# Kernel optimization log

Measured on AMD Instinct MI355X. Metric: run time of the kernel, lower is better.

The kernel has to match this reference:

```python
import jax, jax.numpy as jnp
import numpy as np

B, T, D, H = 4, 1024, 1024, 16
DH = D // H  # 64

def setup_inputs() -> dict:
    key = jax.random.key(0)
    ks = jax.random.split(key, 5)
    s = 1.0 / np.sqrt(D)
    return {
        "x": jax.random.normal(ks[0], (B, T, D), dtype=jnp.float32),
        "Wqkv": jax.random.uniform(ks[1], (D, 3 * D), dtype=jnp.float32, minval=-s, maxval=s),
        "bqkv": jax.random.uniform(ks[2], (3 * D,), dtype=jnp.float32, minval=-s, maxval=s),
        "Wproj": jax.random.uniform(ks[3], (D, D), dtype=jnp.float32, minval=-s, maxval=s),
        "bproj": jax.random.uniform(ks[4], (D,), dtype=jnp.float32, minval=-s, maxval=s),
        "mask": jnp.ones((B, T), dtype=jnp.int32),
    }

def reference(x, Wqkv, bqkv, Wproj, bproj, mask):
    Bx, Tx, C = x.shape
    qkv = x @ Wqkv + bqkv                      # [B,T,3D]
    q, k, v = jnp.split(qkv, 3, axis=-1)
    # [B,H,T,DH]
    q = q.reshape(Bx, Tx, H, DH).transpose(0, 2, 1, 3)
    k = k.reshape(Bx, Tx, H, DH).transpose(0, 2, 1, 3)
    v = v.reshape(Bx, Tx, H, DH).transpose(0, 2, 1, 3)
    att = jnp.einsum("bhqd,bhkd->bhqk", q, k) / np.sqrt(DH)
    causal = jnp.tril(jnp.ones((Tx, Tx), dtype=bool))          # [T,T]
    keep = causal[None, None] & (mask[:, None, None, :] != 0)  # [B,1,T,T] broadcast
    att = jnp.where(keep, att, -jnp.inf)
    att = jax.nn.softmax(att, axis=-1)
    # dropout is identity in eval / p=0
    out = jnp.einsum("bhqk,bhkd->bhqd", att, v)                # [B,H,T,DH]
    out = out.transpose(0, 2, 1, 3).reshape(Bx, Tx, C)
    return out @ Wproj + bproj
```

## Files before the change

### kernel.cpp

```cpp
#include <hip/hip_runtime.h>
#include <hip/hip_bf16.h>
#include <cstddef>
#include <cstdint>

#define Bb 4
#define Tt 1024
#define Dd 1024
#define Hh 16

typedef __bf16 bf16x8 __attribute__((ext_vector_type(8)));
typedef __bf16 bf16x4 __attribute__((ext_vector_type(4)));
typedef float  f32x4  __attribute__((ext_vector_type(4)));

__device__ __forceinline__ void gload16(const void* g, void* l) {
    __builtin_amdgcn_global_load_lds(
        (const __attribute__((address_space(1))) void*)g,
        (__attribute__((address_space(3))) void*)l, 16, 0, 0);
}

__global__ __launch_bounds__(256) void cast_f32_bf16(const float* __restrict__ in,
                                                     __bf16* __restrict__ out, int n4) {
    int i = blockIdx.x * 256 + threadIdx.x;
    if (i < n4) {
        float4 v = ((const float4*)in)[i];
        bf16x4 o = { (__bf16)v.x, (__bf16)v.y, (__bf16)v.z, (__bf16)v.w };
        ((bf16x4*)out)[i] = o;
    }
}

__global__ __launch_bounds__(256) void transpose_cast(const float* __restrict__ in,
                                                      __bf16* __restrict__ out,
                                                      int K, int N) {
    __shared__ float ld[64][65];
    const int k0 = blockIdx.x * 64;
    const int n0 = blockIdx.y * 64;
    #pragma unroll
    for (int i = 0; i < 16; i++) {
        int idx = i * 256 + threadIdx.x;
        int r = idx >> 6, c = idx & 63;
        ld[r][c] = in[(size_t)(k0 + r) * N + n0 + c];
    }
    __syncthreads();
    #pragma unroll
    for (int i = 0; i < 16; i++) {
        int idx = i * 256 + threadIdx.x;
        int r = idx >> 6, c = idx & 63;
        out[(size_t)(n0 + r) * K + k0 + c] = (__bf16)ld[c][r];
    }
}

__global__ __launch_bounds__(256) void gemm_bf16(const __bf16* __restrict__ A,
                                                 const __bf16* __restrict__ Bt,
                                                 const float* __restrict__ bias,
                                                 void* __restrict__ Cout,
                                                 __bf16* __restrict__ vtout,
                                                 int M, int N, int K, int mode) {
    __shared__ __align__(16) __bf16 As[128 * 32];
    __shared__ __align__(16) __bf16 Bs[128 * 32];
    const int tid  = threadIdx.x;
    const int lane = tid & 63;
    const int wave = tid >> 6;
    const int wy = wave >> 1, wx = wave & 1;
    const int l15 = lane & 15, quad = lane >> 4;
    const size_t row0 = (size_t)blockIdx.y * 128;
    const size_t col0 = (size_t)blockIdx.x * 128;

    f32x4 acc[4][4] = {};

    for (int k0 = 0; k0 < K; k0 += 32) {
        #pragma unroll
        for (int i = 0; i < 2; i++) {
            int chunk = i * 256 + tid;
            int r = chunk >> 2, seg = chunk & 3;
            gload16(&A[(row0 + r) * K + k0 + seg * 8], &As[chunk * 8]);
        }
        #pragma unroll
        for (int i = 0; i < 2; i++) {
            int chunk = i * 256 + tid;
            int r = chunk >> 2, seg = chunk & 3;
            gload16(&Bt[(col0 + r) * K + k0 + seg * 8], &Bs[chunk * 8]);
        }
        __syncthreads();
        bf16x8 af[4], bfr[4];
        #pragma unroll
        for (int i = 0; i < 4; i++)
            af[i] = *(const bf16x8*)&As[(wy * 64 + i * 16 + l15) * 32 + quad * 8];
        #pragma unroll
        for (int j = 0; j < 4; j++)
            bfr[j] = *(const bf16x8*)&Bs[(wx * 64 + j * 16 + l15) * 32 + quad * 8];
        #pragma unroll
        for (int i = 0; i < 4; i++)
            #pragma unroll
            for (int j = 0; j < 4; j++)
                acc[i][j] = __builtin_amdgcn_mfma_f32_16x16x32_bf16(af[i], bfr[j], acc[i][j], 0, 0, 0);
        __syncthreads();
    }

    #pragma unroll
    for (int j = 0; j < 4; j++) {
        const size_t col = col0 + wx * 64 + j * 16 + l15;
        const float bj = bias[col];
        const float scale = (mode == 1 && col < 1024) ? 0.125f : 1.0f;
        #pragma unroll
        for (int i = 0; i < 4; i++) {
            const size_t row = row0 + wy * 64 + i * 16 + quad * 4;
            #pragma unroll
            for (int r = 0; r < 4; r++) {
                float v = (acc[i][j][r] + bj) * scale;
                if (mode == 1) {
                    __bf16 bv_ = (__bf16)v;
                    ((__bf16*)Cout)[(row + r) * N + col] = bv_;
                    if (col >= 2048) {
                        size_t rw = row + r;
                        int bidx = (int)(rw >> 10), t = (int)(rw & 1023);
                        int hd = (int)col - 2048;
                        vtout[((size_t)((bidx * Hh + (hd >> 6)) * 64 + (hd & 63))) * Tt + t] = bv_;
                    }
                } else {
                    ((float*)Cout)[(row + r) * N + col] = v;
                }
            }
        }
    }
}

__global__ __launch_bounds__(256) void gemm_bf16_n64(const __bf16* __restrict__ A,
                                                     const __bf16* __restrict__ Bt,
                                                     const float* __restrict__ bias,
                                                     float* __restrict__ Cout,
                                                     int M, int N, int K) {
    __shared__ __align__(16) __bf16 As[128 * 32];
    __shared__ __align__(16) __bf16 Bs[64 * 32];
    const int tid  = threadIdx.x;
    const int lane = tid & 63;
    const int wave = tid >> 6;
    const int wy = wave >> 1, wx = wave & 1;
    const int l15 = lane & 15, quad = lane >> 4;
    const size_t row0 = (size_t)blockIdx.y * 128;
    const size_t col0 = (size_t)blockIdx.x * 64;

    f32x4 acc[4][2] = {};

    for (int k0 = 0; k0 < K; k0 += 32) {
        #pragma unroll
        for (int i = 0; i < 2; i++) {
            int chunk = i * 256 + tid;
            int r = chunk >> 2, seg = chunk & 3;
            gload16(&A[(row0 + r) * K + k0 + seg * 8], &As[chunk * 8]);
        }
        {
            int chunk = tid;
            int r = chunk >> 2, seg = chunk & 3;
            gload16(&Bt[(col0 + r) * K + k0 + seg * 8], &Bs[chunk * 8]);
        }
        __syncthreads();
        bf16x8 af[4], bfr[2];
        #pragma unroll
        for (int i = 0; i < 4; i++)
            af[i] = *(const bf16x8*)&As[(wy * 64 + i * 16 + l15) * 32 + quad * 8];
        #pragma unroll
        for (int j = 0; j < 2; j++)
            bfr[j] = *(const bf16x8*)&Bs[(wx * 32 + j * 16 + l15) * 32 + quad * 8];
        #pragma unroll
        for (int i = 0; i < 4; i++)
            #pragma unroll
            for (int j = 0; j < 2; j++)
                acc[i][j] = __builtin_amdgcn_mfma_f32_16x16x32_bf16(af[i], bfr[j], acc[i][j], 0, 0, 0);
        __syncthreads();
    }

    #pragma unroll
    for (int j = 0; j < 2; j++) {
        const size_t col = col0 + wx * 32 + j * 16 + l15;
        const float bj = bias[col];
        #pragma unroll
        for (int i = 0; i < 4; i++) {
            const size_t row = row0 + wy * 64 + i * 16 + quad * 4;
            #pragma unroll
            for (int r = 0; r < 4; r++)
                Cout[(row + r) * N + col] = acc[i][j][r] + bj;
        }
    }
}

__global__ __launch_bounds__(256, 2) void attn_mfma(const __bf16* __restrict__ qkv,
                                                    const __bf16* __restrict__ vt,
                                                    const int* __restrict__ mask,
                                                    __bf16* __restrict__ att) {
    __shared__ __align__(16) __bf16 Qs[128 * 64];
    __shared__ __align__(16) __bf16 Ks[2][64 * 64];
    __shared__ __align__(16) __bf16 Vs[2][64 * 64];
    __shared__ __align__(16) __bf16 Ps[4][16 * 64];

    const int p = blockIdx.x, h = blockIdx.y, b = blockIdx.z;
    const int qlo = p, qhi = 15 - p, nk = 16 - p;
    const int tid = threadIdx.x, lane = tid & 63, wave = tid >> 6;
    const int l15 = lane & 15, quad = lane >> 4;

    #pragma unroll
    for (int i = 0; i < 4; i++) {
        int c = i * 256 + tid;
        int rr = c >> 3, ch = c & 7;
        int w_ = rr >> 5, s_ = (rr >> 4) & 1, r16 = rr & 15;
        int grow = (s_ ? qhi : qlo) * 64 + w_ * 16 + r16;
        gload16(&qkv[((size_t)(b * Tt + grow)) * 3072 + h * 64 + ((ch ^ (rr & 7)) * 8)],
                &Qs[c * 8]);
    }
    #pragma unroll
    for (int i = 0; i < 2; i++) {
        int c = i * 256 + tid;
        int rr = c >> 3, ch = c & 7, sw = (ch ^ (rr & 7)) * 8;
        gload16(&qkv[((size_t)(b * Tt + rr)) * 3072 + 1024 + h * 64 + sw], &Ks[0][c * 8]);
        gload16(&vt[((size_t)((b * Hh + h) * 64 + rr)) * Tt + sw], &Vs[0][c * 8]);
    }

    f32x4 Oacc[2][4] = {};
    f32x4 lacc[2] = {};
    bf16x8 ones;
    #pragma unroll
    for (int i = 0; i < 8; i++) ones[i] = (__bf16)1.0f;

    for (int kt = 0; kt < nk; kt++) {
        __syncthreads();
        const int cur = kt & 1;
        if (kt + 1 < nk) {
            #pragma unroll
            for (int i = 0; i < 2; i++) {
                int c = i * 256 + tid;
                int rr = c >> 3, ch = c & 7, sw = (ch ^ (rr & 7)) * 8;
                gload16(&qkv[((size_t)(b * Tt + (kt + 1) * 64 + rr)) * 3072 + 1024 + h * 64 + sw],
                        &Ks[cur ^ 1][c * 8]);
                gload16(&vt[((size_t)((b * Hh + h) * 64 + rr)) * Tt + (kt + 1) * 64 + sw],
                        &Vs[cur ^ 1][c * 8]);
            }
        }
        int mv[4];
        #pragma unroll
        for (int j = 0; j < 4; j++) mv[j] = mask[b * Tt + kt * 64 + j * 16 + l15];

        bf16x8 bk[4][2], bv[4][2];
        #pragma unroll
        for (int j = 0; j < 4; j++)
            #pragma unroll
            for (int kc = 0; kc < 2; kc++) {
                int sw = ((kc * 4 + quad) ^ (l15 & 7)) * 8;
                bk[j][kc] = *(const bf16x8*)&Ks[cur][(j * 16 + l15) * 64 + sw];
                bv[j][kc] = *(const bf16x8*)&Vs[cur][(j * 16 + l15) * 64 + sw];
            }

        #pragma unroll
        for (int s = 1; s >= 0; s--) {
            if (s == 0 && kt > qlo) continue;
            const int tile = s ? qhi : qlo;
            const int rowbase = wave * 32 + s * 16;
            bf16x8 aq0 = *(const bf16x8*)&Qs[(rowbase + l15) * 64 + ((quad ^ (l15 & 7)) * 8)];
            bf16x8 aq1 = *(const bf16x8*)&Qs[(rowbase + l15) * 64 + (((4 + quad) ^ (l15 & 7)) * 8)];
            #pragma unroll
            for (int j = 0; j < 4; j++) {
                f32x4 sa = {};
                sa = __builtin_amdgcn_mfma_f32_16x16x32_bf16(aq0, bk[j][0], sa, 0, 0, 0);
                sa = __builtin_amdgcn_mfma_f32_16x16x32_bf16(aq1, bk[j][1], sa, 0, 0, 0);
                #pragma unroll
                for (int r = 0; r < 4; r++) {
                    bool keep = (mv[j] != 0);
                    if (kt == tile) keep = keep && (j * 16 + l15 <= wave * 16 + quad * 4 + r);
                    float pe = keep ? __expf(sa[r]) : 0.0f;
                    int row = quad * 4 + r;
                    int chs = ((j * 2 + (l15 >> 3)) ^ (row & 7)) * 8 + (l15 & 7);
                    Ps[wave][row * 64 + chs] = (__bf16)pe;
                }
            }
            bf16x8 ap0 = *(const bf16x8*)&Ps[wave][l15 * 64 + ((quad ^ (l15 & 7)) * 8)];
            bf16x8 ap1 = *(const bf16x8*)&Ps[wave][l15 * 64 + (((4 + quad) ^ (l15 & 7)) * 8)];
            #pragma unroll
            for (int n = 0; n < 4; n++) {
                Oacc[s][n] = __builtin_amdgcn_mfma_f32_16x16x32_bf16(ap0, bv[n][0], Oacc[s][n], 0, 0, 0);
                Oacc[s][n] = __builtin_amdgcn_mfma_f32_16x16x32_bf16(ap1, bv[n][1], Oacc[s][n], 0, 0, 0);
            }
            lacc[s] = __builtin_amdgcn_mfma_f32_16x16x32_bf16(ap0, ones, lacc[s], 0, 0, 0);
            lacc[s] = __builtin_amdgcn_mfma_f32_16x16x32_bf16(ap1, ones, lacc[s], 0, 0, 0);
        }
    }

    #pragma unroll
    for (int s = 0; s < 2; s++) {
        const int tile = s ? qhi : qlo;
        #pragma unroll
        for (int r = 0; r < 4; r++) {
            const int grow = tile * 64 + wave * 16 + quad * 4 + r;
            const float inv = 1.0f / lacc[s][r];
            #pragma unroll
            for (int n = 0; n < 4; n++)
                att[((size_t)(b * Tt + grow)) * Dd + h * 64 + n * 16 + l15] =
                    (__bf16)(Oacc[s][n][r] * inv);
        }
    }
}

extern "C" void kernel_launch(void* const* d_in, const int* in_sizes, int n_in,
                              void* d_out, int out_size, void* d_ws, size_t ws_size,
                              hipStream_t stream) {
    const float* x     = (const float*)d_in[0];
    const float* Wqkv  = (const float*)d_in[1];
    const float* bqkv  = (const float*)d_in[2];
    const float* Wproj = (const float*)d_in[3];
    const float* bproj = (const float*)d_in[4];
    const int*   mask  = (const int*)d_in[5];
    float* out = (float*)d_out;

    __bf16* xb  = (__bf16*)d_ws;
    __bf16* wqT = xb  + (size_t)4096 * 1024;
    __bf16* wpT = wqT + (size_t)3072 * 1024;
    __bf16* qkv = wpT + (size_t)1024 * 1024;
    __bf16* vt  = qkv + (size_t)4096 * 3072;
    __bf16* att = vt  + (size_t)4 * 16 * 64 * 1024;

    cast_f32_bf16<<<4096, 256, 0, stream>>>(x, xb, (4096 * 1024) / 4);
    transpose_cast<<<dim3(16, 48), 256, 0, stream>>>(Wqkv, wqT, 1024, 3072);
    transpose_cast<<<dim3(16, 16), 256, 0, stream>>>(Wproj, wpT, 1024, 1024);

    gemm_bf16<<<dim3(24, 32), 256, 0, stream>>>(xb, wqT, bqkv, qkv, vt, 4096, 3072, 1024, 1);

    attn_mfma<<<dim3(8, 16, 4), 256, 0, stream>>>(qkv, vt, mask, att);

    gemm_bf16_n64<<<dim3(16, 32), 256, 0, stream>>>(att, wpT, bproj, out, 4096, 1024, 1024);
}
```

Measured before the change: 186.7 us.

## Widen GEMM K-tile with swizzled LDS, split V transpose, transpose attention MFMAs

Both GEMMs now stage 64-wide K tiles in XOR-swizzled LDS. This halves the barrier count per K and avoids bank conflicts on the fragment reads. The scattered V-transpose stores move out of the QKV GEMM epilogue into a separate LDS-tiled transpose kernel. The attention kernel swaps MFMA operand order so P stays in row layout, replaces the ones-matrix MFMA row sum with a register sum plus shuffles, and uses vector mask loads and vector output stores. These changes add one kernel launch and double LDS use in the GEMMs.

```diff
diff --git a/kernel.cpp b/kernel.cpp
--- a/kernel.cpp
+++ b/kernel.cpp
@@ -49,14 +49,36 @@
     }
 }
 
+__global__ __launch_bounds__(256) void v_transpose(const __bf16* __restrict__ qkv,
+                                                   __bf16* __restrict__ vt) {
+    __shared__ __bf16 ld[64][65];
+    const int t0 = blockIdx.x * 64;
+    const int h  = blockIdx.y;
+    const int b  = blockIdx.z;
+    const size_t src = ((size_t)(b * Tt + t0)) * 3072 + 2048 + h * 64;
+    #pragma unroll
+    for (int i = 0; i < 16; i++) {
+        int idx = i * 256 + threadIdx.x;
+        int tr = idx >> 6, dc = idx & 63;
+        ld[tr][dc] = qkv[src + (size_t)tr * 3072 + dc];
+    }
+    __syncthreads();
+    const size_t dst = ((size_t)((b * Hh + h) * 64)) * Tt + t0;
+    #pragma unroll
+    for (int i = 0; i < 16; i++) {
+        int idx = i * 256 + threadIdx.x;
+        int dr = idx >> 6, tc = idx & 63;
+        vt[dst + (size_t)dr * Tt + tc] = ld[tc][dr];
+    }
+}
+
 __global__ __launch_bounds__(256) void gemm_bf16(const __bf16* __restrict__ A,
                                                  const __bf16* __restrict__ Bt,
                                                  const float* __restrict__ bias,
                                                  void* __restrict__ Cout,
-                                                 __bf16* __restrict__ vtout,
                                                  int M, int N, int K, int mode) {
-    __shared__ __align__(16) __bf16 As[128 * 32];
-    __shared__ __align__(16) __bf16 Bs[128 * 32];
+    __shared__ __align__(16) __bf16 As[128 * 64];
+    __shared__ __align__(16) __bf16 Bs[128 * 64];
     const int tid  = threadIdx.x;
     const int lane = tid & 63;
     const int wave = tid >> 6;
@@ -67,32 +89,37 @@
 
     f32x4 acc[4][4] = {};
 
-    for (int k0 = 0; k0 < K; k0 += 32) {
-        #pragma unroll
-        for (int i = 0; i < 2; i++) {
-            int chunk = i * 256 + tid;
-            int r = chunk >> 2, seg = chunk & 3;
-            gload16(&A[(row0 + r) * K + k0 + seg * 8], &As[chunk * 8]);
-        }
-        #pragma unroll
-        for (int i = 0; i < 2; i++) {
-            int chunk = i * 256 + tid;
-            int r = chunk >> 2, seg = chunk & 3;
-            gload16(&Bt[(col0 + r) * K + k0 + seg * 8], &Bs[chunk * 8]);
-        }
-        __syncthreads();
-        bf16x8 af[4], bfr[4];
-        #pragma unroll
-        for (int i = 0; i < 4; i++)
-            af[i] = *(const bf16x8*)&As[(wy * 64 + i * 16 + l15) * 32 + quad * 8];
-        #pragma unroll
-        for (int j = 0; j < 4; j++)
-            bfr[j] = *(const bf16x8*)&Bs[(wx * 64 + j * 16 + l15) * 32 + quad * 8];
-        #pragma unroll
-        for (int i = 0; i < 4; i++)
+    for (int k0 = 0; k0 < K; k0 += 64) {
+        #pragma unroll
+        for (int i = 0; i < 4; i++) {
+            int c = i * 256 + tid;
+            int r = c >> 3, seg = (c & 7) ^ (r & 7);
+            gload16(&A[(row0 + r) * K + k0 + seg * 8], &As[c * 8]);
+        }
+        #pragma unroll
+        for (int i = 0; i < 4; i++) {
+            int c = i * 256 + tid;
+            int r = c >> 3, seg = (c & 7) ^ (r & 7);
+            gload16(&Bt[(col0 + r) * K + k0 + seg * 8], &Bs[c * 8]);
+        }
+        __syncthreads();
+        #pragma unroll
+        for (int kc = 0; kc < 2; kc++) {
+            bf16x8 af[4], bfr[4];
+            #pragma unroll
+            for (int i = 0; i < 4; i++)
+                af[i] = *(const bf16x8*)&As[(wy * 64 + i * 16 + l15) * 64 +
+                                            (((kc * 4 + quad) ^ (l15 & 7)) * 8)];
             #pragma unroll
             for (int j = 0; j < 4; j++)
-                acc[i][j] = __builtin_amdgcn_mfma_f32_16x16x32_bf16(af[i], bfr[j], acc[i][j], 0, 0, 0);
+                bfr[j] = *(const bf16x8*)&Bs[(wx * 64 + j * 16 + l15) * 64 +
+                                             (((kc * 4 + quad) ^ (l15 & 7)) * 8)];
+            #pragma unroll
+            for (int i = 0; i < 4; i++)
+                #pragma unroll
+                for (int j = 0; j < 4; j++)
+                    acc[i][j] = __builtin_amdgcn_mfma_f32_16x16x32_bf16(af[i], bfr[j], acc[i][j], 0, 0, 0);
+        }
         __syncthreads();
     }
 
@@ -107,18 +134,8 @@
             #pragma unroll
             for (int r = 0; r < 4; r++) {
                 float v = (acc[i][j][r] + bj) * scale;
-                if (mode == 1) {
-                    __bf16 bv_ = (__bf16)v;
-                    ((__bf16*)Cout)[(row + r) * N + col] = bv_;
-                    if (col >= 2048) {
-                        size_t rw = row + r;
-                        int bidx = (int)(rw >> 10), t = (int)(rw & 1023);
-                        int hd = (int)col - 2048;
-                        vtout[((size_t)((bidx * Hh + (hd >> 6)) * 64 + (hd & 63))) * Tt + t] = bv_;
-                    }
-                } else {
-                    ((float*)Cout)[(row + r) * N + col] = v;
-                }
+                if (mode == 1) ((__bf16*)Cout)[(row + r) * N + col] = (__bf16)v;
+                else           ((float*)Cout)[(row + r) * N + col] = v;
             }
         }
     }
@@ -129,8 +146,8 @@
                                                      const float* __restrict__ bias,
                                                      float* __restrict__ Cout,
                                                      int M, int N, int K) {
-    __shared__ __align__(16) __bf16 As[128 * 32];
-    __shared__ __align__(16) __bf16 Bs[64 * 32];
+    __shared__ __align__(16) __bf16 As[128 * 64];
+    __shared__ __align__(16) __bf16 Bs[64 * 64];
     const int tid  = threadIdx.x;
     const int lane = tid & 63;
     const int wave = tid >> 6;
@@ -141,31 +158,37 @@
 
     f32x4 acc[4][2] = {};
 
-    for (int k0 = 0; k0 < K; k0 += 32) {
+    for (int k0 = 0; k0 < K; k0 += 64) {
+        #pragma unroll
+        for (int i = 0; i < 4; i++) {
+            int c = i * 256 + tid;
+            int r = c >> 3, seg = (c & 7) ^ (r & 7);
+            gload16(&A[(row0 + r) * K + k0 + seg * 8], &As[c * 8]);
+        }
         #pragma unroll
         for (int i = 0; i < 2; i++) {
-            int chunk = i * 256 + tid;
-            int r = chunk >> 2, seg = chunk & 3;
-            gload16(&A[(row0 + r) * K + k0 + seg * 8], &As[chunk * 8]);
-        }
-        {
-            int chunk = tid;
-            int r = chunk >> 2, seg = chunk & 3;
-            gload16(&Bt[(col0 + r) * K + k0 + seg * 8], &Bs[chunk * 8]);
-        }
-        __syncthreads();
-        bf16x8 af[4], bfr[2];
-        #pragma unroll
-        for (int i = 0; i < 4; i++)
-            af[i] = *(const bf16x8*)&As[(wy * 64 + i * 16 + l15) * 32 + quad * 8];
-        #pragma unroll
-        for (int j = 0; j < 2; j++)
-            bfr[j] = *(const bf16x8*)&Bs[(wx * 32 + j * 16 + l15) * 32 + quad * 8];
-        #pragma unroll
-        for (int i = 0; i < 4; i++)
+            int c = i * 256 + tid;
+            int r = c >> 3, seg = (c & 7) ^ (r & 7);
+            gload16(&Bt[(col0 + r) * K + k0 + seg * 8], &Bs[c * 8]);
+        }
+        __syncthreads();
+        #pragma unroll
+        for (int kc = 0; kc < 2; kc++) {
+            bf16x8 af[4], bfr[2];
+            #pragma unroll
+            for (int i = 0; i < 4; i++)
+                af[i] = *(const bf16x8*)&As[(wy * 64 + i * 16 + l15) * 64 +
+                                            (((kc * 4 + quad) ^ (l15 & 7)) * 8)];
             #pragma unroll
             for (int j = 0; j < 2; j++)
-                acc[i][j] = __builtin_amdgcn_mfma_f32_16x16x32_bf16(af[i], bfr[j], acc[i][j], 0, 0, 0);
+                bfr[j] = *(const bf16x8*)&Bs[(wx * 32 + j * 16 + l15) * 64 +
+                                             (((kc * 4 + quad) ^ (l15 & 7)) * 8)];
+            #pragma unroll
+            for (int i = 0; i < 4; i++)
+                #pragma unroll
+                for (int j = 0; j < 2; j++)
+                    acc[i][j] = __builtin_amdgcn_mfma_f32_16x16x32_bf16(af[i], bfr[j], acc[i][j], 0, 0, 0);
+        }
         __syncthreads();
     }
 
@@ -209,16 +232,13 @@
     #pragma unroll
     for (int i = 0; i < 2; i++) {
         int c = i * 256 + tid;
-        int rr = c >> 3, ch = c & 7, sw = (ch ^ (rr & 7)) * 8;
+        int rr = c >> 3, ch = c & 7, sw = ((ch ^ (rr & 7)) * 8);
         gload16(&qkv[((size_t)(b * Tt + rr)) * 3072 + 1024 + h * 64 + sw], &Ks[0][c * 8]);
         gload16(&vt[((size_t)((b * Hh + h) * 64 + rr)) * Tt + sw], &Vs[0][c * 8]);
     }
 
     f32x4 Oacc[2][4] = {};
-    f32x4 lacc[2] = {};
-    bf16x8 ones;
-    #pragma unroll
-    for (int i = 0; i < 8; i++) ones[i] = (__bf16)1.0f;
+    float lsum[2] = { 0.0f, 0.0f };
 
     for (int kt = 0; kt < nk; kt++) {
         __syncthreads();
@@ -227,25 +247,29 @@
             #pragma unroll
             for (int i = 0; i < 2; i++) {
                 int c = i * 256 + tid;
-                int rr = c >> 3, ch = c & 7, sw = (ch ^ (rr & 7)) * 8;
+                int rr = c >> 3, ch = c & 7, sw = ((ch ^ (rr & 7)) * 8);
                 gload16(&qkv[((size_t)(b * Tt + (kt + 1) * 64 + rr)) * 3072 + 1024 + h * 64 + sw],
                         &Ks[cur ^ 1][c * 8]);
                 gload16(&vt[((size_t)((b * Hh + h) * 64 + rr)) * Tt + (kt + 1) * 64 + sw],
                         &Vs[cur ^ 1][c * 8]);
             }
         }
-        int mv[4];
-        #pragma unroll
-        for (int j = 0; j < 4; j++) mv[j] = mask[b * Tt + kt * 64 + j * 16 + l15];
-
-        bf16x8 bk[4][2], bv[4][2];
+
+        int mv4[4][4];
+        #pragma unroll
+        for (int j = 0; j < 4; j++) {
+            const int4 m4 = *(const int4*)&mask[b * Tt + kt * 64 + j * 16 + quad * 4];
+            mv4[j][0] = m4.x; mv4[j][1] = m4.y; mv4[j][2] = m4.z; mv4[j][3] = m4.w;
+        }
+
+        bf16x8 ak[4][2], av[4][2];
         #pragma unroll
         for (int j = 0; j < 4; j++)
             #pragma unroll
             for (int kc = 0; kc < 2; kc++) {
-                int sw = ((kc * 4 + quad) ^ (l15 & 7)) * 8;
-                bk[j][kc] = *(const bf16x8*)&Ks[cur][(j * 16 + l15) * 64 + sw];
-                bv[j][kc] = *(const bf16x8*)&Vs[cur][(j * 16 + l15) * 64 + sw];
+                int sw = (((kc * 4 + quad) ^ (l15 & 7)) * 8);
+                ak[j][kc] = *(const bf16x8*)&Ks[cur][(j * 16 + l15) * 64 + sw];
+                av[j][kc] = *(const bf16x8*)&Vs[cur][(j * 16 + l15) * 64 + sw];
             }
 
         #pragma unroll
@@ -253,46 +277,50 @@
             if (s == 0 && kt > qlo) continue;
             const int tile = s ? qhi : qlo;
             const int rowbase = wave * 32 + s * 16;
-            bf16x8 aq0 = *(const bf16x8*)&Qs[(rowbase + l15) * 64 + ((quad ^ (l15 & 7)) * 8)];
-            bf16x8 aq1 = *(const bf16x8*)&Qs[(rowbase + l15) * 64 + (((4 + quad) ^ (l15 & 7)) * 8)];
+            bf16x8 q0 = *(const bf16x8*)&Qs[(rowbase + l15) * 64 + ((quad ^ (l15 & 7)) * 8)];
+            bf16x8 q1 = *(const bf16x8*)&Qs[(rowbase + l15) * 64 + (((4 + quad) ^ (l15 & 7)) * 8)];
+
             #pragma unroll
             for (int j = 0; j < 4; j++) {
-                f32x4 sa = {};
-                sa = __builtin_amdgcn_mfma_f32_16x16x32_bf16(aq0, bk[j][0], sa, 0, 0, 0);
-                sa = __builtin_amdgcn_mfma_f32_16x16x32_bf16(aq1, bk[j][1], sa, 0, 0, 0);
+                f32x4 st = {};
+                st = __builtin_amdgcn_mfma_f32_16x16x32_bf16(ak[j][0], q0, st, 0, 0, 0);
+                st = __builtin_amdgcn_mfma_f32_16x16x32_bf16(ak[j][1], q1, st, 0, 0, 0);
+                bf16x4 pv;
                 #pragma unroll
                 for (int r = 0; r < 4; r++) {
-                    bool keep = (mv[j] != 0);
-                    if (kt == tile) keep = keep && (j * 16 + l15 <= wave * 16 + quad * 4 + r);
-                    float pe = keep ? __expf(sa[r]) : 0.0f;
-                    int row = quad * 4 + r;
-                    int chs = ((j * 2 + (l15 >> 3)) ^ (row & 7)) * 8 + (l15 & 7);
-                    Ps[wave][row * 64 + chs] = (__bf16)pe;
+                    const int tloc = j * 16 + quad * 4 + r;
+                    bool keep = (mv4[j][r] != 0);
+                    if (kt == tile) keep = keep && (tloc <= wave * 16 + l15);
+                    const float pe = keep ? __expf(st[r]) : 0.0f;
+                    lsum[s] += pe;
+                    pv[r] = (__bf16)pe;
                 }
-            }
-            bf16x8 ap0 = *(const bf16x8*)&Ps[wave][l15 * 64 + ((quad ^ (l15 & 7)) * 8)];
-            bf16x8 ap1 = *(const bf16x8*)&Ps[wave][l15 * 64 + (((4 + quad) ^ (l15 & 7)) * 8)];
+                *(bf16x4*)&Ps[wave][l15 * 64 + (((j * 4 + quad) ^ ((l15 & 7) << 1)) * 4)] = pv;
+            }
+            bf16x8 p0 = *(const bf16x8*)&Ps[wave][l15 * 64 + (((2 * quad) ^ ((l15 & 7) << 1)) * 4)];
+            bf16x8 p1 = *(const bf16x8*)&Ps[wave][l15 * 64 + (((2 * (4 + quad)) ^ ((l15 & 7) << 1)) * 4)];
             #pragma unroll
             for (int n = 0; n < 4; n++) {
-                Oacc[s][n] = __builtin_amdgcn_mfma_f32_16x16x32_bf16(ap0, bv[n][0], Oacc[s][n], 0, 0, 0);
-                Oacc[s][n] = __builtin_amdgcn_mfma_f32_16x16x32_bf16(ap1, bv[n][1], Oacc[s][n], 0, 0, 0);
-            }
-            lacc[s] = __builtin_amdgcn_mfma_f32_16x16x32_bf16(ap0, ones, lacc[s], 0, 0, 0);
-            lacc[s] = __builtin_amdgcn_mfma_f32_16x16x32_bf16(ap1, ones, lacc[s], 0, 0, 0);
+                Oacc[s][n] = __builtin_amdgcn_mfma_f32_16x16x32_bf16(av[n][0], p0, Oacc[s][n], 0, 0, 0);
+                Oacc[s][n] = __builtin_amdgcn_mfma_f32_16x16x32_bf16(av[n][1], p1, Oacc[s][n], 0, 0, 0);
+            }
         }
     }
 
     #pragma unroll
     for (int s = 0; s < 2; s++) {
         const int tile = s ? qhi : qlo;
-        #pragma unroll
-        for (int r = 0; r < 4; r++) {
-            const int grow = tile * 64 + wave * 16 + quad * 4 + r;
-            const float inv = 1.0f / lacc[s][r];
-            #pragma unroll
-            for (int n = 0; n < 4; n++)
-                att[((size_t)(b * Tt + grow)) * Dd + h * 64 + n * 16 + l15] =
-                    (__bf16)(Oacc[s][n][r] * inv);
+        float lt = lsum[s];
+        lt += __shfl_xor(lt, 16);
+        lt += __shfl_xor(lt, 32);
+        const float inv = 1.0f / lt;
+        const int q = tile * 64 + wave * 16 + l15;
+        #pragma unroll
+        for (int n = 0; n < 4; n++) {
+            bf16x4 o;
+            #pragma unroll
+            for (int r = 0; r < 4; r++) o[r] = (__bf16)(Oacc[s][n][r] * inv);
+            *(bf16x4*)&att[((size_t)(b * Tt + q)) * Dd + h * 64 + n * 16 + quad * 4] = o;
         }
     }
 }
@@ -319,8 +347,9 @@
     transpose_cast<<<dim3(16, 48), 256, 0, stream>>>(Wqkv, wqT, 1024, 3072);
     transpose_cast<<<dim3(16, 16), 256, 0, stream>>>(Wproj, wpT, 1024, 1024);
 
-    gemm_bf16<<<dim3(24, 32), 256, 0, stream>>>(xb, wqT, bqkv, qkv, vt, 4096, 3072, 1024, 1);
-
+    gemm_bf16<<<dim3(24, 32), 256, 0, stream>>>(xb, wqT, bqkv, qkv, 4096, 3072, 1024, 1);
+
+    v_transpose<<<dim3(16, 16, 4), 256, 0, stream>>>(qkv, vt);
     attn_mfma<<<dim3(8, 16, 4), 256, 0, stream>>>(qkv, vt, mask, att);
 
     gemm_bf16_n64<<<dim3(16, 32), 256, 0, stream>>>(att, wpT, bproj, out, 4096, 1024, 1024);
```

After: 176.2 us. -5.6%, faster.
